# Kernel tuning notes

Measured on AMD Instinct MI355X. Metric: run time of the kernel, lower is better.

Reference implementation:

```python
import jax, jax.numpy as jnp
import numpy as np

B, T, N, D = 16, 12, 1024, 128
M, TOPK = 64, 16


def _ln(x, eps=1e-5):
    mu = x.mean(-1, keepdims=True)
    var = ((x - mu) ** 2).mean(-1, keepdims=True)
    return (x - mu) / jnp.sqrt(var + eps)


def setup_inputs() -> dict:
    key = jax.random.key(0)
    ks = jax.random.split(key, 18)
    s = 1.0 / np.sqrt(D)
    inp = {
        "x": jax.random.normal(ks[0], (B, T, N, D), jnp.float32),
        "eigvec": jax.random.normal(ks[1], (D, N, 1), jnp.float32),
        "eigvalue": jax.random.normal(ks[2], (D,), jnp.float32),
        "Wq": jax.random.normal(ks[3], (D, D), jnp.float32) * s,
        "bq": jax.random.normal(ks[4], (D,), jnp.float32) * 0.01,
        "Wk": jax.random.normal(ks[5], (D, D), jnp.float32) * s,
        "bk": jax.random.normal(ks[6], (D,), jnp.float32) * 0.01,
        "Wv": jax.random.normal(ks[7], (D, D), jnp.float32) * s,
        "bv": jax.random.normal(ks[8], (D,), jnp.float32) * 0.01,
        "Wo": jax.random.normal(ks[9], (D, D), jnp.float32) * s,
        "bo": jax.random.normal(ks[10], (D,), jnp.float32) * 0.01,
        "node_emb": jax.random.normal(ks[11], (M, 2 * D), jnp.float32),
        "ffW1": jax.random.normal(ks[12], (D, D), jnp.float32) * s,
        "ffb1": jax.random.normal(ks[13], (D,), jnp.float32) * 0.01,
        "ffW2": jax.random.normal(ks[14], (D, D), jnp.float32) * s,
        "ffb2": jax.random.normal(ks[15], (D,), jnp.float32) * 0.01,
        "adj": jax.random.randint(ks[16], (N, 16), 0, N),
    }
    return inp


def reference(x, eigvec, eigvalue, Wq, bq, Wk, bk, Wv, bv, Wo, bo,
              node_emb, ffW1, ffb1, ffW2, ffb2, adj):
    # spectral positional term: [N,D] = eigvec^T scaled per-column by eigvalue
    x_ = x + eigvec[:, :, 0].T * eigvalue  # [B,T,N,D]

    Q = x_ @ Wq + bq
    K = x_ @ Wk + bk
    V = x_ @ Wv + bv

    # node selection: memory embeddings attend over concat(Q,K) features
    nodevec3 = jnp.concatenate([Q, K], axis=-1)  # [B,T,N,2D]
    supports2 = jax.nn.softmax(jnp.einsum('me,btne->btmn', node_emb, nodevec3), axis=-1)
    _, idx = jax.lax.top_k(supports2, TOPK)  # idx: [B,T,M,TOPK]
    idx_flat = idx.reshape(B, T, M * TOPK)

    def gather(t):  # t: [B,T,N,D] -> [B,T,M,TOPK,D]
        return jnp.take_along_axis(t, idx_flat[..., None], axis=2).reshape(B, T, M, TOPK, D)

    selQ, selK, selV = gather(Q), gather(K), gather(V)

    attn = jax.nn.softmax(
        jnp.einsum('btmkd,btmjd->btmkj', selQ, selK) / np.sqrt(D), axis=-1)
    node_new = jnp.einsum('btmkj,btmjd->btmkd', attn, selV).reshape(B, T, M * TOPK, D)

    # scatter_add aggregation back to the N nodes, normalized by hit counts
    b_ix = jnp.arange(B)[:, None, None]
    t_ix = jnp.arange(T)[None, :, None]
    dict1 = jnp.zeros((B, T, N, D), x.dtype).at[b_ix, t_ix, idx_flat].add(node_new)
    counts = jnp.full((B, T, N), 1e-14, x.dtype).at[b_ix, t_ix, idx_flat].add(1.0)
    value = dict1 / counts[..., None]

    value = (value @ Wo + bo) + x_
    value = _ln(value)
    h = jax.nn.relu(value @ ffW1 + ffb1) @ ffW2 + ffb2
    return _ln(h + value)
```

## Files before the change

### kernel.cpp

```cpp
#include <hip/hip_runtime.h>
#include <math.h>

#define RTOT   196608
#define NNODE  1024
#define NBT    192

typedef __attribute__((ext_vector_type(8))) short short8;
typedef __attribute__((ext_vector_type(4))) float f32x4;

__device__ __forceinline__ unsigned short f2bf(float f) {
  unsigned u = __float_as_uint(f);
  return (unsigned short)((u + 0x7fffu + ((u >> 16) & 1u)) >> 16);
}
__device__ __forceinline__ float bf2f(unsigned short b) {
  return __uint_as_float(((unsigned)b) << 16);
}

__global__ __launch_bounds__(256) void pos_kernel(
    const float* __restrict__ eigvec, const float* __restrict__ eigval,
    float* __restrict__ pos) {
  int i = blockIdx.x * 256 + threadIdx.x;
  int d = i >> 10, n = i & 1023;
  pos[n * 128 + d] = eigvec[d * 1024 + n] * eigval[d];
}

__global__ __launch_bounds__(256) void prepw_kernel(
    const float* __restrict__ W0, const float* __restrict__ W1,
    const float* __restrict__ W2, const float* __restrict__ W3,
    const float* __restrict__ W4, const float* __restrict__ W5,
    unsigned short* __restrict__ out) {
  int i = blockIdx.x * 256 + threadIdx.x;
  int wsel = i >> 14, rem = i & 16383, c = rem >> 7, k = rem & 127;
  const float* W = (wsel == 0) ? W0 : (wsel == 1) ? W1 : (wsel == 2) ? W2
                 : (wsel == 3) ? W3 : (wsel == 4) ? W4 : W5;
  out[i] = f2bf(W[k * 128 + c]);
}

__global__ __launch_bounds__(256) void wcomb_kernel(
    const float* __restrict__ Wq, const float* __restrict__ Wk,
    const float* __restrict__ bq, const float* __restrict__ bk,
    const float* __restrict__ emb, float* __restrict__ Wcomb,
    float* __restrict__ bcomb) {
  int i = blockIdx.x * 256 + threadIdx.x;
  if (i < 8192) {
    int k = i >> 6, m = i & 63;
    float s = 0.f;
    for (int d = 0; d < 128; ++d)
      s += Wq[k * 128 + d] * emb[m * 256 + d]
         + Wk[k * 128 + d] * emb[m * 256 + 128 + d];
    Wcomb[i] = s;
  } else if (i < 8256) {
    int m = i - 8192;
    float s = 0.f;
    for (int d = 0; d < 128; ++d)
      s += bq[d] * emb[m * 256 + d] + bk[d] * emb[m * 256 + 128 + d];
    bcomb[m] = s;
  }
}

template<int NCOL, int KCHUNKS, int ADDPOS, int HASBIAS, int WRITEXB>
__global__ __launch_bounds__(256, 2) void gemm_k(
    const float* __restrict__ A1, const float* __restrict__ A2,
    const float* __restrict__ W, const float* __restrict__ bias,
    const float* __restrict__ pos, unsigned short* __restrict__ xb,
    float* __restrict__ out) {
  __shared__ float As[128 * 64];
  __shared__ float Ws[64 * NCOL];
  constexpr int JW = (NCOL == 128) ? 2 : 1;
  const int tid = threadIdx.x;
  const int tx = tid & 15, ty = tid >> 4;
  const int row0 = blockIdx.x * 128;

  float acc[8][4 * JW];
#pragma unroll
  for (int i = 0; i < 8; ++i)
#pragma unroll
    for (int j = 0; j < 4 * JW; ++j) acc[i][j] = 0.f;

  for (int kc = 0; kc < KCHUNKS; ++kc) {
    const int kt = kc * 64;
    const float* __restrict__ Asrc = (kt < 128) ? A1 : A2;
    const int kbase = kt & 127;
#pragma unroll
    for (int i = 0; i < 8; ++i) {
      int f = tid + 256 * i;
      int m = f >> 4;
      int k4 = (f & 15) << 2;
      int r = row0 + m;
      float4 a = *(const float4*)&Asrc[(size_t)r * 128 + kbase + k4];
      if constexpr (ADDPOS) {
        float4 p = *(const float4*)&pos[(r & 1023) * 128 + kbase + k4];
        a.x += p.x; a.y += p.y; a.z += p.z; a.w += p.w;
      }
      if constexpr (WRITEXB) {
        unsigned lo = (unsigned)f2bf(a.x) | ((unsigned)f2bf(a.y) << 16);
        unsigned hi = (unsigned)f2bf(a.z) | ((unsigned)f2bf(a.w) << 16);
        *(uint2*)&xb[(size_t)r * 128 + kbase + k4] = make_uint2(lo, hi);
      }
      *(float4*)&As[m * 64 + k4] = a;
    }
#pragma unroll
    for (int i = 0; i < NCOL / 16; ++i) {
      int f = tid + 256 * i;
      int kk = f / (NCOL / 4);
      int c4 = (f % (NCOL / 4)) << 2;
      *(float4*)&Ws[kk * NCOL + c4] =
          *(const float4*)&W[(size_t)(kt + kk) * NCOL + c4];
    }
    __syncthreads();
    for (int k4 = 0; k4 < 64; k4 += 4) {
      float a[8][4];
#pragma unroll
      for (int i = 0; i < 8; ++i)
        *(float4*)&a[i][0] = *(const float4*)&As[(ty * 8 + i) * 64 + k4];
#pragma unroll
      for (int kk = 0; kk < 4; ++kk) {
        float4 w0 = *(const float4*)&Ws[(k4 + kk) * NCOL + tx * 4];
        float4 w1;
        if constexpr (JW == 2)
          w1 = *(const float4*)&Ws[(k4 + kk) * NCOL + 64 + tx * 4];
#pragma unroll
        for (int i = 0; i < 8; ++i) {
          float av = a[i][kk];
          acc[i][0] = fmaf(av, w0.x, acc[i][0]);
          acc[i][1] = fmaf(av, w0.y, acc[i][1]);
          acc[i][2] = fmaf(av, w0.z, acc[i][2]);
          acc[i][3] = fmaf(av, w0.w, acc[i][3]);
          if constexpr (JW == 2) {
            acc[i][4] = fmaf(av, w1.x, acc[i][4]);
            acc[i][5] = fmaf(av, w1.y, acc[i][5]);
            acc[i][6] = fmaf(av, w1.z, acc[i][6]);
            acc[i][7] = fmaf(av, w1.w, acc[i][7]);
          }
        }
      }
    }
    __syncthreads();
  }
  float4 b0 = make_float4(0.f, 0.f, 0.f, 0.f);
  float4 b1 = make_float4(0.f, 0.f, 0.f, 0.f);
  if constexpr (HASBIAS) {
    b0 = *(const float4*)&bias[tx * 4];
    if constexpr (JW == 2) b1 = *(const float4*)&bias[64 + tx * 4];
  }
#pragma unroll
  for (int i = 0; i < 8; ++i) {
    const int r = row0 + ty * 8 + i;
    {
      float4 o = make_float4(acc[i][0] + b0.x, acc[i][1] + b0.y,
                             acc[i][2] + b0.z, acc[i][3] + b0.w);
      *(float4*)&out[(size_t)r * NCOL + tx * 4] = o;
    }
    if constexpr (JW == 2) {
      float4 o = make_float4(acc[i][4] + b1.x, acc[i][5] + b1.y,
                             acc[i][6] + b1.z, acc[i][7] + b1.w);
      *(float4*)&out[(size_t)r * NCOL + 64 + tx * 4] = o;
    }
  }
}

__global__ __launch_bounds__(256, 2) void gemm_qkv(
    const unsigned short* __restrict__ A, const unsigned short* __restrict__ Wt,
    const float* __restrict__ bq, const float* __restrict__ bk,
    const float* __restrict__ bv,
    unsigned short* __restrict__ outq, unsigned short* __restrict__ outk,
    unsigned short* __restrict__ outv) {
  const int tid = threadIdx.x;
  const int w = tid >> 6, lane = tid & 63;
  const int wr = w >> 1, wc = w & 1;
  const int lhi = lane >> 4, llo = lane & 15;
  const int r0 = blockIdx.x * 128;

  short8 af[4][4];
#pragma unroll
  for (int i = 0; i < 4; ++i)
#pragma unroll
    for (int kq = 0; kq < 4; ++kq)
      af[i][kq] = *(const short8*)&A[(size_t)(r0 + wr * 64 + i * 16 + llo) * 128 +
                                     kq * 32 + lhi * 8];
#pragma unroll
  for (int s = 0; s < 3; ++s) {
    const unsigned short* __restrict__ Bt = Wt + s * 16384;
    const float* __restrict__ bias = (s == 0) ? bq : (s == 1) ? bk : bv;
    unsigned short* __restrict__ outb = (s == 0) ? outq : (s == 1) ? outk : outv;

    short8 bf[4][4];
#pragma unroll
    for (int j = 0; j < 4; ++j)
#pragma unroll
      for (int kq = 0; kq < 4; ++kq)
        bf[j][kq] = *(const short8*)&Bt[(size_t)(wc * 64 + j * 16 + llo) * 128 +
                                        kq * 32 + lhi * 8];
    f32x4 acc[4][4];
#pragma unroll
    for (int i = 0; i < 4; ++i)
#pragma unroll
      for (int j = 0; j < 4; ++j) acc[i][j] = (f32x4)(0.0f);
#pragma unroll
    for (int i = 0; i < 4; ++i)
#pragma unroll
      for (int kq = 0; kq < 4; ++kq)
#pragma unroll
        for (int j = 0; j < 4; ++j)
          acc[i][j] = __builtin_amdgcn_mfma_f32_16x16x32_bf16(
              af[i][kq], bf[j][kq], acc[i][j], 0, 0, 0);

    float bvals[4];
#pragma unroll
    for (int j = 0; j < 4; ++j) bvals[j] = bias[wc * 64 + j * 16 + llo];
#pragma unroll
    for (int i = 0; i < 4; ++i)
#pragma unroll
      for (int reg = 0; reg < 4; ++reg) {
        const int r = r0 + wr * 64 + i * 16 + lhi * 4 + reg;
#pragma unroll
        for (int j = 0; j < 4; ++j) {
          const int c = wc * 64 + j * 16 + llo;
          outb[(size_t)r * 128 + c] = f2bf(acc[i][j][reg] + bvals[j]);
        }
      }
  }
}

template<int EPI>
__global__ __launch_bounds__(256, 2) void gemm_mfma(
    const unsigned short* __restrict__ A, const unsigned short* __restrict__ Bt,
    const float* __restrict__ bias, const float* __restrict__ x,
    const float* __restrict__ pos, const unsigned short* __restrict__ resb,
    float* __restrict__ outf, unsigned short* __restrict__ outb) {
  __shared__ float lds_s[128][2];
  __shared__ float lds_q[128][2];
  const int tid = threadIdx.x;
  const int w = tid >> 6, lane = tid & 63;
  const int wr = w >> 1, wc = w & 1;
  const int lhi = lane >> 4, llo = lane & 15;
  const int r0 = blockIdx.x * 128;

  short8 bf[4][4];
#pragma unroll
  for (int j = 0; j < 4; ++j)
#pragma unroll
    for (int kq = 0; kq < 4; ++kq)
      bf[j][kq] = *(const short8*)&Bt[(size_t)(wc * 64 + j * 16 + llo) * 128 +
                                      kq * 32 + lhi * 8];
  f32x4 acc[4][4];
#pragma unroll
  for (int i = 0; i < 4; ++i)
#pragma unroll
    for (int j = 0; j < 4; ++j) acc[i][j] = (f32x4)(0.0f);

#pragma unroll
  for (int i = 0; i < 4; ++i) {
    short8 af[4];
#pragma unroll
    for (int kq = 0; kq < 4; ++kq)
      af[kq] = *(const short8*)&A[(size_t)(r0 + wr * 64 + i * 16 + llo) * 128 +
                                  kq * 32 + lhi * 8];
#pragma unroll
    for (int kq = 0; kq < 4; ++kq)
#pragma unroll
      for (int j = 0; j < 4; ++j)
        acc[i][j] = __builtin_amdgcn_mfma_f32_16x16x32_bf16(
            af[kq], bf[j][kq], acc[i][j], 0, 0, 0);
  }

  float bvals[4];
#pragma unroll
  for (int j = 0; j < 4; ++j) bvals[j] = bias[wc * 64 + j * 16 + llo];

  if constexpr (EPI == 1 || EPI == 3) {
#pragma unroll
    for (int i = 0; i < 4; ++i) {
#pragma unroll
      for (int reg = 0; reg < 4; ++reg) {
        const int rl = wr * 64 + i * 16 + lhi * 4 + reg;
        const int r = r0 + rl;
        float s = 0.f, q = 0.f;
#pragma unroll
        for (int j = 0; j < 4; ++j) {
          const int c = wc * 64 + j * 16 + llo;
          float vv = acc[i][j][reg] + bvals[j];
          if constexpr (EPI == 1)
            vv += x[(size_t)r * 128 + c] + pos[(r & 1023) * 128 + c];
          else
            vv += bf2f(resb[(size_t)r * 128 + c]);
          acc[i][j][reg] = vv;
          s += vv; q += vv * vv;
        }
#pragma unroll
        for (int m = 1; m < 16; m <<= 1) {
          s += __shfl_xor(s, m);
          q += __shfl_xor(q, m);
        }
        if (llo == 0) { lds_s[rl][wc] = s; lds_q[rl][wc] = q; }
      }
    }
    __syncthreads();
#pragma unroll
    for (int i = 0; i < 4; ++i) {
#pragma unroll
      for (int reg = 0; reg < 4; ++reg) {
        const int rl = wr * 64 + i * 16 + lhi * 4 + reg;
        const int r = r0 + rl;
        float s = lds_s[rl][0] + lds_s[rl][1];
        float q = lds_q[rl][0] + lds_q[rl][1];
        float mu = s * (1.f / 128.f);
        float rstd = rsqrtf(q * (1.f / 128.f) - mu * mu + 1e-5f);
#pragma unroll
        for (int j = 0; j < 4; ++j) {
          const int c = wc * 64 + j * 16 + llo;
          float vv = (acc[i][j][reg] - mu) * rstd;
          if constexpr (EPI == 1)
            outb[(size_t)r * 128 + c] = f2bf(vv);
          else
            outf[(size_t)r * 128 + c] = vv;
        }
      }
    }
  } else {
#pragma unroll
    for (int i = 0; i < 4; ++i)
#pragma unroll
      for (int reg = 0; reg < 4; ++reg) {
        const int rl = wr * 64 + i * 16 + lhi * 4 + reg;
        const int r = r0 + rl;
#pragma unroll
        for (int j = 0; j < 4; ++j) {
          const int c = wc * 64 + j * 16 + llo;
          float vv = acc[i][j][reg] + bvals[j];
          if constexpr (EPI == 2) {
            vv = fmaxf(vv, 0.f);
            outb[(size_t)r * 128 + c] = f2bf(vv);
          } else {
            outf[(size_t)r * 128 + c] = vv;
          }
        }
      }
  }
}

__global__ __launch_bounds__(256) void topk_kernel(
    const float* __restrict__ S, int* __restrict__ idx_out) {
  __shared__ float sc[8 * 1088];
  __shared__ int cnt[8];
  const int tid = threadIdx.x;
  const int bt = blockIdx.x >> 3, mg = blockIdx.x & 7;
  if (tid < 8) cnt[tid] = 0;
#pragma unroll
  for (int u = 0; u < 8; ++u) {
    int f = tid + 256 * u;
    int n = f >> 1, half = f & 1;
    float4 v = *(const float4*)&S[((size_t)bt * 1024 + n) * 64 + mg * 8 + half * 4];
    int p = (n >> 4) * 17 + (n & 15);
    sc[(half * 4 + 0) * 1088 + p] = v.x;
    sc[(half * 4 + 1) * 1088 + p] = v.y;
    sc[(half * 4 + 2) * 1088 + p] = v.z;
    sc[(half * 4 + 3) * 1088 + p] = v.w;
  }
  __syncthreads();
  const int lane = tid & 63, w = tid >> 6;
  for (int h2 = 0; h2 < 2; ++h2) {
    const int ml = w * 2 + h2;
    float ov[16], r[16];
#pragma unroll
    for (int j = 0; j < 16; ++j) {
      float t = sc[ml * 1088 + lane * 17 + j];
      ov[j] = t; r[j] = t;
    }
#pragma unroll
    for (int k = 2; k <= 16; k <<= 1) {
#pragma unroll
      for (int d = k >> 1; d >= 1; d >>= 1) {
#pragma unroll
        for (int i = 0; i < 16; ++i) {
          int j = i ^ d;
          if (j > i) {
            bool up = ((i & k) == 0);
            float a = r[i], b = r[j];
            float mn = fminf(a, b), mx = fmaxf(a, b);
            r[i] = up ? mn : mx;
            r[j] = up ? mx : mn;
          }
        }
      }
    }
#pragma unroll
    for (int md = 1; md < 64; md <<= 1) {
      float c[16];
#pragma unroll
      for (int i = 0; i < 16; ++i)
        c[i] = fmaxf(r[i], __shfl_xor(r[15 - i], md));
#pragma unroll
      for (int d = 8; d >= 1; d >>= 1) {
#pragma unroll
        for (int i = 0; i < 16; ++i) {
          int j = i ^ d;
          if (j > i) {
            float a = c[i], b = c[j];
            c[i] = fminf(a, b);
            c[j] = fmaxf(a, b);
          }
        }
      }
#pragma unroll
      for (int i = 0; i < 16; ++i) r[i] = c[i];
    }
    const float tstar = r[0];
    const int outbase = (bt * 64 + mg * 8 + ml) << 4;
#pragma unroll
    for (int j = 0; j < 16; ++j) {
      if (ov[j] >= tstar) {
        int s = atomicAdd(&cnt[ml], 1);
        if (s < 16) idx_out[outbase + s] = lane * 16 + j;
      }
    }
  }
}

__global__ __launch_bounds__(256) void attn_dense(
    const unsigned short* __restrict__ Q, const unsigned short* __restrict__ K,
    const unsigned short* __restrict__ V, const int* __restrict__ idx,
    unsigned short* __restrict__ node_new) {
  __shared__ float sQ[16 * 132], sK[16 * 132], sV[16 * 132];
  __shared__ float sP[16 * 16];
  __shared__ int sidx[16];
  const int tid = threadIdx.x;
  const int bt = blockIdx.x >> 6, m = blockIdx.x & 63;
  if (tid < 16) sidx[tid] = idx[((bt * 64 + m) << 4) + tid];
  __syncthreads();
  const size_t base = (size_t)bt * 1024 * 128;
#pragma unroll
  for (int u = 0; u < 3; ++u) {
    int f = tid + 256 * u;
    int mat = f >> 8;
    int rem = f & 255;
    int r = rem >> 4;
    int c8 = (rem & 15) << 3;
    const unsigned short* src = (mat == 0) ? Q : (mat == 1) ? K : V;
    float* dst = (mat == 0) ? sQ : (mat == 1) ? sK : sV;
    uint4 raw = *(const uint4*)&src[base + (size_t)sidx[r] * 128 + c8];
    float4 f0 = make_float4(bf2f(raw.x & 0xffff), bf2f(raw.x >> 16),
                            bf2f(raw.y & 0xffff), bf2f(raw.y >> 16));
    float4 f1 = make_float4(bf2f(raw.z & 0xffff), bf2f(raw.z >> 16),
                            bf2f(raw.w & 0xffff), bf2f(raw.w >> 16));
    *(float4*)&dst[r * 132 + c8] = f0;
    *(float4*)&dst[r * 132 + c8 + 4] = f1;
  }
  __syncthreads();
  const int kk = tid >> 4, jj = tid & 15;
  float s = 0.f;
#pragma unroll
  for (int c4 = 0; c4 < 128; c4 += 4) {
    float4 q = *(const float4*)&sQ[kk * 132 + c4];
    float4 kv = *(const float4*)&sK[jj * 132 + c4];
    s = fmaf(q.x, kv.x, s); s = fmaf(q.y, kv.y, s);
    s = fmaf(q.z, kv.z, s); s = fmaf(q.w, kv.w, s);
  }
  s *= 0.08838834764831845f;
  float mx = s;
#pragma unroll
  for (int off = 8; off >= 1; off >>= 1) mx = fmaxf(mx, __shfl_xor(mx, off, 16));
  float e = expf(s - mx);
  float sum = e;
#pragma unroll
  for (int off = 8; off >= 1; off >>= 1) sum += __shfl_xor(sum, off, 16);
  sP[kk * 16 + jj] = e / sum;
  __syncthreads();
  const int dc = tid & 15;
  const int d0 = dc * 8;
  float o[8] = {0.f, 0.f, 0.f, 0.f, 0.f, 0.f, 0.f, 0.f};
#pragma unroll
  for (int j = 0; j < 16; ++j) {
    float p = sP[kk * 16 + j];
    float4 v0 = *(const float4*)&sV[j * 132 + d0];
    float4 v1 = *(const float4*)&sV[j * 132 + d0 + 4];
    o[0] = fmaf(p, v0.x, o[0]); o[1] = fmaf(p, v0.y, o[1]);
    o[2] = fmaf(p, v0.z, o[2]); o[3] = fmaf(p, v0.w, o[3]);
    o[4] = fmaf(p, v1.x, o[4]); o[5] = fmaf(p, v1.y, o[5]);
    o[6] = fmaf(p, v1.z, o[6]); o[7] = fmaf(p, v1.w, o[7]);
  }
  unsigned short* orow = node_new + base + (size_t)(m * 16 + kk) * 128 + d0;
  uint4 st;
  st.x = (unsigned)f2bf(o[0]) | ((unsigned)f2bf(o[1]) << 16);
  st.y = (unsigned)f2bf(o[2]) | ((unsigned)f2bf(o[3]) << 16);
  st.z = (unsigned)f2bf(o[4]) | ((unsigned)f2bf(o[5]) << 16);
  st.w = (unsigned)f2bf(o[6]) | ((unsigned)f2bf(o[7]) << 16);
  *(uint4*)orow = st;
}

__global__ __launch_bounds__(256) void build_lists(
    const int* __restrict__ idx, int* __restrict__ lists,
    int* __restrict__ counts) {
  int i = blockIdx.x * 256 + threadIdx.x;
  int bt = i >> 10, j = i & 1023;
  int n = idx[i];
  int slot = atomicAdd(&counts[bt * 1024 + n], 1);
  lists[(size_t)(bt * 1024 + n) * 64 + slot] = j;
}

__global__ __launch_bounds__(256) void gather_sum(
    const unsigned short* __restrict__ node_new, const int* __restrict__ lists,
    const int* __restrict__ counts, unsigned short* __restrict__ outb) {
  const int lane = threadIdx.x & 63;
  const int row = blockIdx.x * 4 + (threadIdx.x >> 6);
  const int cnt = counts[row];
  const int bt = row >> 10;
  const float inv = 1.0f / ((float)cnt + 1e-14f);
  const int* lp = lists + (size_t)row * 64;
  float ax = 0.f, ay = 0.f;
  for (int j = 0; j < cnt; ++j) {
    int src = lp[j];
    unsigned u = *(const unsigned*)&node_new[((size_t)bt * 1024 + src) * 128 + lane * 2];
    ax += bf2f(u & 0xffff); ay += bf2f(u >> 16);
  }
  ax *= inv; ay *= inv;
  unsigned pk = (unsigned)f2bf(ax) | ((unsigned)f2bf(ay) << 16);
  *(unsigned*)&outb[(size_t)row * 128 + lane * 2] = pk;
}

extern "C" void kernel_launch(void* const* d_in, const int* in_sizes, int n_in,
                              void* d_out, int out_size, void* d_ws, size_t ws_size,
                              hipStream_t stream) {
  const float* x      = (const float*)d_in[0];
  const float* eigvec = (const float*)d_in[1];
  const float* eigval = (const float*)d_in[2];
  const float* Wq     = (const float*)d_in[3];
  const float* bq     = (const float*)d_in[4];
  const float* Wk     = (const float*)d_in[5];
  const float* bk     = (const float*)d_in[6];
  const float* Wv     = (const float*)d_in[7];
  const float* bv     = (const float*)d_in[8];
  const float* Wo     = (const float*)d_in[9];
  const float* bo     = (const float*)d_in[10];
  const float* nemb   = (const float*)d_in[11];
  const float* ffW1   = (const float*)d_in[12];
  const float* ffb1   = (const float*)d_in[13];
  const float* ffW2   = (const float*)d_in[14];
  const float* ffb2   = (const float*)d_in[15];
  float* outp = (float*)d_out;

  char* ws = (char*)d_ws;
  float*          pos    = (float*)(ws + 0);
  int*            idxp   = (int*)  (ws + 524288);
  int*            counts = (int*)  (ws + 1310720);
  float*          Wcomb  = (float*)(ws + 1310720);
  float*          bcomb  = (float*)(ws + 1343488);
  unsigned short* Wtall  = (unsigned short*)(ws + 2097152);
  unsigned short* xb     = (unsigned short*)(ws + 2293760);
  unsigned short* Kb     = (unsigned short*)(ws + 52625408);
  unsigned short* Vb     = (unsigned short*)(ws + 102957056);
  float*          Sbuf   = (float*)(ws + 153288704);
  unsigned short* Wt_o = Wtall + 49152;
  unsigned short* Wt_1 = Wtall + 65536;
  unsigned short* Wt_2 = Wtall + 81920;
  unsigned short* vln  = xb;
  unsigned short* h1   = Kb;
  int*            lists = (int*)Vb;
  unsigned short* nnb  = (unsigned short*)Sbuf;
  unsigned short* Qb   = (unsigned short*)d_out;
  unsigned short* dictb = (unsigned short*)d_out;

  pos_kernel<<<512, 256, 0, stream>>>(eigvec, eigval, pos);
  prepw_kernel<<<384, 256, 0, stream>>>(Wq, Wk, Wv, Wo, ffW1, ffW2, Wtall);
  wcomb_kernel<<<33, 256, 0, stream>>>(Wq, Wk, bq, bk, nemb, Wcomb, bcomb);

  gemm_k<64, 2, 1, 1, 1><<<1536, 256, 0, stream>>>(
      x, nullptr, Wcomb, bcomb, pos, xb, Sbuf);
  topk_kernel<<<1536, 256, 0, stream>>>(Sbuf, idxp);

  gemm_qkv<<<1536, 256, 0, stream>>>(xb, Wtall, bq, bk, bv, Qb, Kb, Vb);

  attn_dense<<<12288, 256, 0, stream>>>(Qb, Kb, Vb, idxp, nnb);

  hipMemsetAsync(counts, 0, (size_t)NBT * NNODE * 4, stream);
  build_lists<<<768, 256, 0, stream>>>(idxp, lists, counts);
  gather_sum<<<49152, 256, 0, stream>>>(nnb, lists, counts, dictb);

  gemm_mfma<1><<<1536, 256, 0, stream>>>(
      dictb, Wt_o, bo, x, pos, nullptr, nullptr, vln);
  gemm_mfma<2><<<1536, 256, 0, stream>>>(
      vln, Wt_1, ffb1, nullptr, nullptr, nullptr, nullptr, h1);
  gemm_mfma<3><<<1536, 256, 0, stream>>>(
      h1, Wt_2, ffb2, nullptr, nullptr, vln, outp, nullptr);
}
```

Measured before the change: 600.4 us.

## Fuse QKV projection into attention kernel, computing only selected rows

After: 670.9 us. 1.12x slower.

```diff
diff --git a/kernel.cpp b/kernel.cpp
--- a/kernel.cpp
+++ b/kernel.cpp
@@ -159,69 +159,6 @@
   }
 }
 
-__global__ __launch_bounds__(256, 2) void gemm_qkv(
-    const unsigned short* __restrict__ A, const unsigned short* __restrict__ Wt,
-    const float* __restrict__ bq, const float* __restrict__ bk,
-    const float* __restrict__ bv,
-    unsigned short* __restrict__ outq, unsigned short* __restrict__ outk,
-    unsigned short* __restrict__ outv) {
-  const int tid = threadIdx.x;
-  const int w = tid >> 6, lane = tid & 63;
-  const int wr = w >> 1, wc = w & 1;
-  const int lhi = lane >> 4, llo = lane & 15;
-  const int r0 = blockIdx.x * 128;
-
-  short8 af[4][4];
-#pragma unroll
-  for (int i = 0; i < 4; ++i)
-#pragma unroll
-    for (int kq = 0; kq < 4; ++kq)
-      af[i][kq] = *(const short8*)&A[(size_t)(r0 + wr * 64 + i * 16 + llo) * 128 +
-                                     kq * 32 + lhi * 8];
-#pragma unroll
-  for (int s = 0; s < 3; ++s) {
-    const unsigned short* __restrict__ Bt = Wt + s * 16384;
-    const float* __restrict__ bias = (s == 0) ? bq : (s == 1) ? bk : bv;
-    unsigned short* __restrict__ outb = (s == 0) ? outq : (s == 1) ? outk : outv;
-
-    short8 bf[4][4];
-#pragma unroll
-    for (int j = 0; j < 4; ++j)
-#pragma unroll
-      for (int kq = 0; kq < 4; ++kq)
-        bf[j][kq] = *(const short8*)&Bt[(size_t)(wc * 64 + j * 16 + llo) * 128 +
-                                        kq * 32 + lhi * 8];
-    f32x4 acc[4][4];
-#pragma unroll
-    for (int i = 0; i < 4; ++i)
-#pragma unroll
-      for (int j = 0; j < 4; ++j) acc[i][j] = (f32x4)(0.0f);
-#pragma unroll
-    for (int i = 0; i < 4; ++i)
-#pragma unroll
-      for (int kq = 0; kq < 4; ++kq)
-#pragma unroll
-        for (int j = 0; j < 4; ++j)
-          acc[i][j] = __builtin_amdgcn_mfma_f32_16x16x32_bf16(
-              af[i][kq], bf[j][kq], acc[i][j], 0, 0, 0);
-
-    float bvals[4];
-#pragma unroll
-    for (int j = 0; j < 4; ++j) bvals[j] = bias[wc * 64 + j * 16 + llo];
-#pragma unroll
-    for (int i = 0; i < 4; ++i)
-#pragma unroll
-      for (int reg = 0; reg < 4; ++reg) {
-        const int r = r0 + wr * 64 + i * 16 + lhi * 4 + reg;
-#pragma unroll
-        for (int j = 0; j < 4; ++j) {
-          const int c = wc * 64 + j * 16 + llo;
-          outb[(size_t)r * 128 + c] = f2bf(acc[i][j][reg] + bvals[j]);
-        }
-      }
-  }
-}
-
 template<int EPI>
 __global__ __launch_bounds__(256, 2) void gemm_mfma(
     const unsigned short* __restrict__ A, const unsigned short* __restrict__ Bt,
@@ -417,36 +354,55 @@
   }
 }
 
-__global__ __launch_bounds__(256) void attn_dense(
-    const unsigned short* __restrict__ Q, const unsigned short* __restrict__ K,
-    const unsigned short* __restrict__ V, const int* __restrict__ idx,
+__global__ __launch_bounds__(256) void attn_fused(
+    const unsigned short* __restrict__ xb, const unsigned short* __restrict__ Wt,
+    const float* __restrict__ bq, const float* __restrict__ bk,
+    const float* __restrict__ bv, const int* __restrict__ idx,
     unsigned short* __restrict__ node_new) {
   __shared__ float sQ[16 * 132], sK[16 * 132], sV[16 * 132];
   __shared__ float sP[16 * 16];
   __shared__ int sidx[16];
   const int tid = threadIdx.x;
   const int bt = blockIdx.x >> 6, m = blockIdx.x & 63;
-  if (tid < 16) sidx[tid] = idx[((bt * 64 + m) << 4) + tid];
+  if (tid < 16) sidx[tid] = idx[((bt * 64 + m) << 4) + tid] & 1023;
   __syncthreads();
   const size_t base = (size_t)bt * 1024 * 128;
-#pragma unroll
-  for (int u = 0; u < 3; ++u) {
-    int f = tid + 256 * u;
-    int mat = f >> 8;
-    int rem = f & 255;
-    int r = rem >> 4;
-    int c8 = (rem & 15) << 3;
-    const unsigned short* src = (mat == 0) ? Q : (mat == 1) ? K : V;
-    float* dst = (mat == 0) ? sQ : (mat == 1) ? sK : sV;
-    uint4 raw = *(const uint4*)&src[base + (size_t)sidx[r] * 128 + c8];
-    float4 f0 = make_float4(bf2f(raw.x & 0xffff), bf2f(raw.x >> 16),
-                            bf2f(raw.y & 0xffff), bf2f(raw.y >> 16));
-    float4 f1 = make_float4(bf2f(raw.z & 0xffff), bf2f(raw.z >> 16),
-                            bf2f(raw.w & 0xffff), bf2f(raw.w >> 16));
-    *(float4*)&dst[r * 132 + c8] = f0;
-    *(float4*)&dst[r * 132 + c8 + 4] = f1;
+  const int w = tid >> 6, lane = tid & 63;
+  const int lhi = lane >> 4, llo = lane & 15;
+
+  short8 af[4];
+  const unsigned short* arow = &xb[base + (size_t)sidx[llo] * 128];
+#pragma unroll
+  for (int kq = 0; kq < 4; ++kq)
+    af[kq] = *(const short8*)&arow[kq * 32 + lhi * 8];
+
+#pragma unroll
+  for (int s = 0; s < 3; ++s) {
+    const unsigned short* __restrict__ Bt = Wt + s * 16384;
+    const float* __restrict__ bias = (s == 0) ? bq : (s == 1) ? bk : bv;
+    float* __restrict__ dst = (s == 0) ? sQ : (s == 1) ? sK : sV;
+    f32x4 acc[2];
+    acc[0] = (f32x4)(0.0f);
+    acc[1] = (f32x4)(0.0f);
+#pragma unroll
+    for (int j = 0; j < 2; ++j)
+#pragma unroll
+      for (int kq = 0; kq < 4; ++kq) {
+        short8 bfr = *(const short8*)&Bt[(size_t)(w * 32 + j * 16 + llo) * 128 +
+                                         kq * 32 + lhi * 8];
+        acc[j] = __builtin_amdgcn_mfma_f32_16x16x32_bf16(af[kq], bfr, acc[j], 0, 0, 0);
+      }
+#pragma unroll
+    for (int j = 0; j < 2; ++j) {
+      const int c = w * 32 + j * 16 + llo;
+      const float bb = bias[c];
+#pragma unroll
+      for (int reg = 0; reg < 4; ++reg)
+        dst[(lhi * 4 + reg) * 132 + c] = acc[j][reg] + bb;
+    }
   }
   __syncthreads();
+
   const int kk = tid >> 4, jj = tid & 15;
   float s = 0.f;
 #pragma unroll
@@ -493,8 +449,8 @@
     int* __restrict__ counts) {
   int i = blockIdx.x * 256 + threadIdx.x;
   int bt = i >> 10, j = i & 1023;
-  int n = idx[i];
-  int slot = atomicAdd(&counts[bt * 1024 + n], 1);
+  int n = idx[i] & 1023;
+  int slot = atomicAdd(&counts[bt * 1024 + n], 1) & 63;
   lists[(size_t)(bt * 1024 + n) * 64 + slot] = j;
 }
 
@@ -503,13 +459,13 @@
     const int* __restrict__ counts, unsigned short* __restrict__ outb) {
   const int lane = threadIdx.x & 63;
   const int row = blockIdx.x * 4 + (threadIdx.x >> 6);
-  const int cnt = counts[row];
+  const int cnt = counts[row] & 127;
   const int bt = row >> 10;
   const float inv = 1.0f / ((float)cnt + 1e-14f);
   const int* lp = lists + (size_t)row * 64;
   float ax = 0.f, ay = 0.f;
   for (int j = 0; j < cnt; ++j) {
-    int src = lp[j];
+    int src = lp[j & 63] & 1023;
     unsigned u = *(const unsigned*)&node_new[((size_t)bt * 1024 + src) * 128 + lane * 2];
     ax += bf2f(u & 0xffff); ay += bf2f(u >> 16);
   }
@@ -547,17 +503,15 @@
   float*          bcomb  = (float*)(ws + 1343488);
   unsigned short* Wtall  = (unsigned short*)(ws + 2097152);
   unsigned short* xb     = (unsigned short*)(ws + 2293760);
-  unsigned short* Kb     = (unsigned short*)(ws + 52625408);
-  unsigned short* Vb     = (unsigned short*)(ws + 102957056);
+  unsigned short* h1buf  = (unsigned short*)(ws + 52625408);
+  int*            lists  = (int*)  (ws + 102957056);
   float*          Sbuf   = (float*)(ws + 153288704);
   unsigned short* Wt_o = Wtall + 49152;
   unsigned short* Wt_1 = Wtall + 65536;
   unsigned short* Wt_2 = Wtall + 81920;
   unsigned short* vln  = xb;
-  unsigned short* h1   = Kb;
-  int*            lists = (int*)Vb;
+  unsigned short* h1   = h1buf;
   unsigned short* nnb  = (unsigned short*)Sbuf;
-  unsigned short* Qb   = (unsigned short*)d_out;
   unsigned short* dictb = (unsigned short*)d_out;
 
   pos_kernel<<<512, 256, 0, stream>>>(eigvec, eigval, pos);
@@ -568,9 +522,7 @@
       x, nullptr, Wcomb, bcomb, pos, xb, Sbuf);
   topk_kernel<<<1536, 256, 0, stream>>>(Sbuf, idxp);
 
-  gemm_qkv<<<1536, 256, 0, stream>>>(xb, Wtall, bq, bk, bv, Qb, Kb, Vb);
-
-  attn_dense<<<12288, 256, 0, stream>>>(Qb, Kb, Vb, idxp, nnb);
+  attn_fused<<<12288, 256, 0, stream>>>(xb, Wtall, bq, bk, bv, idxp, nnb);
 
   hipMemsetAsync(counts, 0, (size_t)NBT * NNODE * 4, stream);
   build_lists<<<768, 256, 0, stream>>>(idxp, lists, counts);
```
